# Kernel tuning notes

Measured on AMD Instinct MI355X. Metric: run time of the kernel, lower is better.

## Reference

```python
import jax, jax.numpy as jnp
import numpy as np

B, S, D, H = 16, 512, 768, 12
DH = D // H


def setup_inputs() -> dict:
    key = jax.random.key(0)
    ks = jax.random.split(key, 12)
    hidden_states = jax.random.normal(ks[0], (B, S, D), dtype=jnp.float32)
    # additive padding mask: 0 for valid, -10000 for padded tail tokens
    lengths = jax.random.randint(ks[1], (B,), S // 2, S + 1)
    pad = (jnp.arange(S)[None, :] >= lengths[:, None]).astype(jnp.float32)
    attention_mask = (pad * -10000.0)[:, None, None, :]  # [B,1,1,S]
    # row-stochastic graph prior over codes
    pr = jax.random.uniform(ks[2], (B, S, S), dtype=jnp.float32)
    prior = pr / jnp.sum(pr, axis=-1, keepdims=True)
    s = 0.02
    params = dict(
        Wq=jax.random.normal(ks[3], (D, D)) * s, bq=jnp.zeros((D,)),
        Wk=jax.random.normal(ks[4], (D, D)) * s, bk=jnp.zeros((D,)),
        Wv=jax.random.normal(ks[5], (D, D)) * s, bv=jnp.zeros((D,)),
        Wg=jax.random.normal(ks[6], (D, 2)) * s, bg=jnp.zeros((2,)),
        Wo=jax.random.normal(ks[7], (D, D)) * s, bo=jnp.zeros((D,)),
        gamma=jnp.ones((D,)), beta=jnp.zeros((D,)),
    )
    return dict(hidden_states=hidden_states, attention_mask=attention_mask,
                prior=prior, **params)


def _layer_norm(x, gamma, beta, eps=1e-5):
    mu = jnp.mean(x, axis=-1, keepdims=True)
    var = jnp.mean(jnp.square(x - mu), axis=-1, keepdims=True)
    return (x - mu) * jax.lax.rsqrt(var + eps) * gamma + beta


def reference(hidden_states, attention_mask, prior,
              Wq, bq, Wk, bk, Wv, bv, Wg, bg, Wo, bo, gamma, beta):
    b, s, d = hidden_states.shape
    # project and split heads: [B,S,H,DH]
    q = (hidden_states @ Wq + bq).reshape(b, s, H, DH)
    k = (hidden_states @ Wk + bk).reshape(b, s, H, DH)
    v = (hidden_states @ Wv + bv).reshape(b, s, H, DH)
    scores = jnp.einsum('bshd,bthd->bhst', q, k) / jnp.sqrt(jnp.float32(DH))
    scores = scores + attention_mask  # broadcast [B,1,1,S]
    probs = jax.nn.softmax(scores, axis=-1)  # [B,H,S,S]
    # gate: avg-pool over valid tokens, softmax(linear/2)
    valid = (attention_mask.squeeze((1, 2)) == 0.0).astype(hidden_states.dtype)  # [B,S]
    denom = jnp.maximum(jnp.sum(valid, axis=1, keepdims=True), 1.0)
    h_pool = jnp.sum(hidden_states * valid[:, :, None], axis=1) / denom  # [B,D]
    gate = jax.nn.softmax((h_pool @ Wg + bg) / 2.0, axis=-1)  # [B,2]
    probs = probs * gate[:, 0, None, None, None] + prior[:, None, :, :] * gate[:, 1, None, None, None]
    ctx = jnp.einsum('bhst,bthd->bshd', probs, v).reshape(b, s, d)
    out = jax.nn.relu(ctx @ Wo + bo)
    out = _layer_norm(out + hidden_states, gamma, beta)
    return out
```

## Files before the change

kernel.cpp:

```cpp
#include <hip/hip_runtime.h>

#define NB_ 16
#define S_ 512
#define D_ 768
#define H_ 12
#define DH_ 64
#define QT_ 64
#define KT_ 128
#define LDQ_ 1536

typedef __attribute__((ext_vector_type(8))) short bf16x8;
typedef __attribute__((ext_vector_type(4))) float f32x4;
typedef unsigned short ushort_t;

__device__ __forceinline__ unsigned short f2bf(float f){
  unsigned int u = __float_as_uint(f);
  u += 0x7fffu + ((u >> 16) & 1u);
  return (unsigned short)(u >> 16);
}
__device__ __forceinline__ float bf2f(unsigned short s){
  return __uint_as_float(((unsigned int)s) << 16);
}
__device__ __forceinline__ unsigned int pack2(float a, float b){
  return (unsigned int)f2bf(a) | ((unsigned int)f2bf(b) << 16);
}
__device__ __forceinline__ void gld16(const ushort_t* g, ushort_t* l){
  __builtin_amdgcn_global_load_lds((const __attribute__((address_space(1))) unsigned int*)g,
                                   (__attribute__((address_space(3))) unsigned int*)l, 16, 0, 0);
}

__global__ __launch_bounds__(256) void k_setup(
    const float* __restrict__ hs, const float* __restrict__ mask, const float* __restrict__ prior,
    const float* __restrict__ W0, const float* __restrict__ W1,
    const float* __restrict__ W2, const float* __restrict__ W3,
    const float* __restrict__ b0, const float* __restrict__ b1, const float* __restrict__ b2,
    ushort_t* __restrict__ hsb, ushort_t* __restrict__ wt, float* __restrict__ bqkv,
    float* __restrict__ partial, float* __restrict__ pcnt, ushort_t* __restrict__ priorb)
{
  __shared__ float t[32][33];
  const int bx = blockIdx.x, tid = threadIdx.x;
  if (bx < 512){
    int chunk = bx & 31, b = bx >> 5;
    const float* mrow = mask + b * S_ + chunk * 16;
    const float* base = hs + ((size_t)b * S_ + chunk * 16) * D_;
    ushort_t* obase = hsb + ((size_t)b * S_ + chunk * 16) * D_;
    float a0 = 0.f, a1 = 0.f, a2 = 0.f, cnt = 0.f;
#pragma unroll 2
    for (int s = 0; s < 16; s++){
      const float* r = base + (size_t)s * D_;
      float x0 = r[tid], x1 = r[tid + 256], x2 = r[tid + 512];
      ushort_t* o = obase + (size_t)s * D_;
      o[tid] = f2bf(x0); o[tid + 256] = f2bf(x1); o[tid + 512] = f2bf(x2);
      if (mrow[s] == 0.0f){ a0 += x0; a1 += x1; a2 += x2; cnt += 1.0f; }
    }
    float* o = partial + (size_t)(b * 32 + chunk) * D_;
    o[tid] = a0; o[tid + 256] = a1; o[tid + 512] = a2;
    if (tid == 0) pcnt[b * 32 + chunk] = cnt;
  } else if (bx < 512 + 2304){
    int idx = bx - 512;
    int z = idx / 576, rem = idx - z * 576;
    int ky = rem / 24, nx = rem - ky * 24;
    const float* W = (z == 0) ? W0 : (z == 1) ? W1 : (z == 2) ? W2 : W3;
    ushort_t* o = wt + (size_t)z * D_ * D_;
    int j = tid & 31, i0 = tid >> 5;
    int kb = ky * 32, nb = nx * 32;
#pragma unroll
    for (int r = 0; r < 4; r++){
      int i = i0 + r * 8;
      t[i][j] = W[(size_t)(kb + i) * D_ + nb + j];
    }
    __syncthreads();
#pragma unroll
    for (int r = 0; r < 4; r++){
      int i = i0 + r * 8;
      o[(size_t)(nb + i) * D_ + kb + j] = f2bf(t[j][i]);
    }
  } else if (bx < 2825){
    int i = (bx - 2816) * 256 + tid;
    if (i < 3 * D_){
      float v = (i < D_) ? b0[i] : (i < 2 * D_) ? b1[i - D_] : b2[i - 2 * D_];
      bqkv[i] = v;
    }
  } else {
    size_t i = (size_t)(bx - 2825) * 4096 + (size_t)tid * 16;
    const float4* s4 = (const float4*)(prior + i);
    float4 f0 = s4[0], f1 = s4[1], f2 = s4[2], f3 = s4[3];
    uint4 p0, p1;
    p0.x = pack2(f0.x, f0.y); p0.y = pack2(f0.z, f0.w);
    p0.z = pack2(f1.x, f1.y); p0.w = pack2(f1.z, f1.w);
    p1.x = pack2(f2.x, f2.y); p1.y = pack2(f2.z, f2.w);
    p1.z = pack2(f3.x, f3.y); p1.w = pack2(f3.z, f3.w);
    *(uint4*)(priorb + i) = p0;
    *(uint4*)(priorb + i + 8) = p1;
  }
}

__global__ __launch_bounds__(256, 2) void k_gemm_qkv(
    const ushort_t* __restrict__ Am, const ushort_t* __restrict__ Bm,
    ushort_t* __restrict__ Cq, ushort_t* __restrict__ vtp,
    const float* __restrict__ bias,
    const float* __restrict__ partial, const float* __restrict__ pcnt,
    const float* __restrict__ Wg, const float* __restrict__ bg, float* __restrict__ gate)
{
  __shared__ ushort_t As[2][128 * 64];
  __shared__ ushort_t Bs[2][128 * 64];
  const int tid = threadIdx.x;

  if (blockIdx.y == 18){
    if (blockIdx.x >= 16) return;
    float* red = (float*)As;
    float* hp  = red + 256;
    int b = blockIdx.x;
    float a0 = 0.f, a1 = 0.f, a2 = 0.f;
#pragma unroll
    for (int c = 0; c < 32; c++){
      const float* p = partial + (size_t)(b * 32 + c) * D_;
      a0 += p[tid]; a1 += p[tid + 256]; a2 += p[tid + 512];
    }
    float denom = 0.f;
#pragma unroll
    for (int c = 0; c < 32; c++) denom += pcnt[b * 32 + c];
    float inv = 1.0f / fmaxf(denom, 1.0f);
    hp[tid] = a0 * inv; hp[tid + 256] = a1 * inv; hp[tid + 512] = a2 * inv;
    __syncthreads();
    float p0 = 0.f, p1 = 0.f;
    for (int d = tid; d < D_; d += 256){ p0 += hp[d] * Wg[d * 2]; p1 += hp[d] * Wg[d * 2 + 1]; }
    red[tid] = p0; __syncthreads();
    for (int o = 128; o > 0; o >>= 1){ if (tid < o) red[tid] += red[tid + o]; __syncthreads(); }
    float z0 = red[0]; __syncthreads();
    red[tid] = p1; __syncthreads();
    for (int o = 128; o > 0; o >>= 1){ if (tid < o) red[tid] += red[tid + o]; __syncthreads(); }
    float z1 = red[0];
    if (tid == 0){
      z0 = (z0 + bg[0]) * 0.5f; z1 = (z1 + bg[1]) * 0.5f;
      float m = fmaxf(z0, z1);
      float e0 = __expf(z0 - m), e1 = __expf(z1 - m);
      float ssum = e0 + e1;
      gate[b * 2] = e0 / ssum; gate[b * 2 + 1] = e1 / ssum;
    }
    return;
  }

  const int m0 = blockIdx.x * 128, n0 = blockIdx.y * 128;
  const int wid = tid >> 6, lane = tid & 63;
  const int quad = lane >> 4, l16 = lane & 15;
  const int wm = wid >> 1, wn = wid & 1;
  const int sw = l16 & 7;

  auto stage = [&](int buf, int k0){
#pragma unroll
    for (int c = 0; c < 4; c++){
      int idx = tid + c * 256;
      int row = idx >> 3, p = idx & 7;
      int cg = p ^ (row & 7);
      gld16(Am + (size_t)(m0 + row) * D_ + k0 + cg * 8, &As[buf][idx * 8]);
    }
#pragma unroll
    for (int c = 0; c < 4; c++){
      int idx = tid + c * 256;
      int row = idx >> 3, p = idx & 7;
      int cg = p ^ (row & 7);
      gld16(Bm + (size_t)(n0 + row) * D_ + k0 + cg * 8, &Bs[buf][idx * 8]);
    }
  };

  f32x4 acc[4][4];
#pragma unroll
  for (int i = 0; i < 4; i++)
#pragma unroll
    for (int j = 0; j < 4; j++) acc[i][j] = (f32x4){0.f, 0.f, 0.f, 0.f};

  stage(0, 0);
  int cur = 0;
  for (int k0 = 0; k0 < D_; k0 += 64){
    if (k0 + 64 < D_){
      stage(cur ^ 1, k0 + 64);
      __builtin_amdgcn_sched_barrier(0);
      asm volatile("s_waitcnt vmcnt(8)" ::: "memory");
    } else {
      __builtin_amdgcn_sched_barrier(0);
      asm volatile("s_waitcnt vmcnt(0)" ::: "memory");
    }
    __builtin_amdgcn_sched_barrier(0);
    __builtin_amdgcn_s_barrier();
#pragma unroll
    for (int ks = 0; ks < 2; ks++){
      bf16x8 af[4], bfv[4];
#pragma unroll
      for (int mi = 0; mi < 4; mi++){
        int row = wm * 64 + mi * 16 + l16;
        af[mi] = *(const bf16x8*)(&As[cur][(row * 8 + ((ks * 4 + quad) ^ sw)) * 8]);
      }
#pragma unroll
      for (int ni = 0; ni < 4; ni++){
        int row = wn * 64 + ni * 16 + l16;
        bfv[ni] = *(const bf16x8*)(&Bs[cur][(row * 8 + ((ks * 4 + quad) ^ sw)) * 8]);
      }
      __builtin_amdgcn_s_setprio(1);
#pragma unroll
      for (int mi = 0; mi < 4; mi++)
#pragma unroll
        for (int ni = 0; ni < 4; ni++)
          acc[mi][ni] = __builtin_amdgcn_mfma_f32_16x16x32_bf16(af[mi], bfv[ni], acc[mi][ni], 0, 0, 0);
      __builtin_amdgcn_s_setprio(0);
    }
    __builtin_amdgcn_sched_barrier(0);
    __builtin_amdgcn_s_barrier();
    cur ^= 1;
  }

  if (n0 >= 1536){
    const int bb = m0 >> 9;
#pragma unroll
    for (int mi = 0; mi < 4; mi++){
#pragma unroll
      for (int ni = 0; ni < 4; ni++){
        int col = n0 + wn * 64 + ni * 16 + l16;
        float bcol = bias[col];
        int hh = (col - 1536) >> 6, dh = (col - 1536) & 63;
        int trow = (m0 & 511) + wm * 64 + mi * 16 + quad * 4;
        uint2 pk;
        pk.x = pack2(acc[mi][ni][0] + bcol, acc[mi][ni][1] + bcol);
        pk.y = pack2(acc[mi][ni][2] + bcol, acc[mi][ni][3] + bcol);
        *(uint2*)(vtp + ((size_t)(bb * H_ + hh) * DH_ + dh) * S_ + trow) = pk;
      }
    }
    return;
  }
#pragma unroll
  for (int mi = 0; mi < 4; mi++){
#pragma unroll
    for (int ni = 0; ni < 4; ni++){
      int col = n0 + wn * 64 + ni * 16 + l16;
      float bcol = bias[col];
#pragma unroll
      for (int r = 0; r < 4; r++){
        int row = m0 + wm * 64 + mi * 16 + quad * 4 + r;
        Cq[(size_t)row * LDQ_ + col] = f2bf(acc[mi][ni][r] + bcol);
      }
    }
  }
}

template<int OUTBF16, int RELU, int RESID, int MAP>
__global__ __launch_bounds__(256, 2) void k_gemm_bt(
    const ushort_t* __restrict__ Am, long sA, int lda,
    const ushort_t* __restrict__ Bm, long sB, int ldb,
    void* __restrict__ Cp, long sC, int ldc,
    const float* __restrict__ bias,
    const float* __restrict__ resid, int K)
{
  __shared__ ushort_t As[2][128 * 64];
  __shared__ ushort_t Bs[2][128 * 64];
  int z, bm, bn;
  if (MAP == 2){ z = blockIdx.x; bm = blockIdx.y; bn = blockIdx.z; }
  else if (MAP == 1){ z = blockIdx.z; bm = blockIdx.x; bn = blockIdx.y; }
  else { z = blockIdx.z; bm = blockIdx.y; bn = blockIdx.x; }
  const ushort_t* Ab = Am + (size_t)z * sA;
  const ushort_t* Bb = Bm + (size_t)z * sB;
  const long coff = (long)z * sC;
  const int tid = threadIdx.x;
  const int m0 = bm * 128, n0 = bn * 128;
  const int wid = tid >> 6, lane = tid & 63;
  const int quad = lane >> 4, l16 = lane & 15;
  const int wm = wid >> 1, wn = wid & 1;
  const int sw = l16 & 7;

  auto stage = [&](int buf, int k0){
#pragma unroll
    for (int c = 0; c < 4; c++){
      int idx = tid + c * 256;
      int row = idx >> 3, p = idx & 7;
      int cg = p ^ (row & 7);
      gld16(Ab + (size_t)(m0 + row) * lda + k0 + cg * 8, &As[buf][idx * 8]);
    }
#pragma unroll
    for (int c = 0; c < 4; c++){
      int idx = tid + c * 256;
      int row = idx >> 3, p = idx & 7;
      int cg = p ^ (row & 7);
      gld16(Bb + (size_t)(n0 + row) * ldb + k0 + cg * 8, &Bs[buf][idx * 8]);
    }
  };

  f32x4 acc[4][4];
#pragma unroll
  for (int i = 0; i < 4; i++)
#pragma unroll
    for (int j = 0; j < 4; j++) acc[i][j] = (f32x4){0.f, 0.f, 0.f, 0.f};

  stage(0, 0);
  int cur = 0;
  for (int k0 = 0; k0 < K; k0 += 64){
    if (k0 + 64 < K){
      stage(cur ^ 1, k0 + 64);
      __builtin_amdgcn_sched_barrier(0);
      asm volatile("s_waitcnt vmcnt(8)" ::: "memory");
    } else {
      __builtin_amdgcn_sched_barrier(0);
      asm volatile("s_waitcnt vmcnt(0)" ::: "memory");
    }
    __builtin_amdgcn_sched_barrier(0);
    __builtin_amdgcn_s_barrier();
#pragma unroll
    for (int ks = 0; ks < 2; ks++){
      bf16x8 af[4], bfv[4];
#pragma unroll
      for (int mi = 0; mi < 4; mi++){
        int row = wm * 64 + mi * 16 + l16;
        af[mi] = *(const bf16x8*)(&As[cur][(row * 8 + ((ks * 4 + quad) ^ sw)) * 8]);
      }
#pragma unroll
      for (int ni = 0; ni < 4; ni++){
        int row = wn * 64 + ni * 16 + l16;
        bfv[ni] = *(const bf16x8*)(&Bs[cur][(row * 8 + ((ks * 4 + quad) ^ sw)) * 8]);
      }
      __builtin_amdgcn_s_setprio(1);
#pragma unroll
      for (int mi = 0; mi < 4; mi++)
#pragma unroll
        for (int ni = 0; ni < 4; ni++)
          acc[mi][ni] = __builtin_amdgcn_mfma_f32_16x16x32_bf16(af[mi], bfv[ni], acc[mi][ni], 0, 0, 0);
      __builtin_amdgcn_s_setprio(0);
    }
    __builtin_amdgcn_sched_barrier(0);
    __builtin_amdgcn_s_barrier();
    cur ^= 1;
  }

#pragma unroll
  for (int mi = 0; mi < 4; mi++){
#pragma unroll
    for (int ni = 0; ni < 4; ni++){
      int col = n0 + wn * 64 + ni * 16 + l16;
      float bcol = bias ? bias[col] : 0.0f;
#pragma unroll
      for (int r = 0; r < 4; r++){
        int row = m0 + wm * 64 + mi * 16 + quad * 4 + r;
        float v = acc[mi][ni][r] + bcol;
        if (RELU) v = fmaxf(v, 0.0f);
        if (RESID) v += resid[(size_t)row * ldc + col];
        long idx = coff + (long)row * ldc + col;
        if (OUTBF16) ((ushort_t*)Cp)[idx] = f2bf(v);
        else         ((float*)Cp)[idx] = v;
      }
    }
  }
}

__global__ __launch_bounds__(256) void k_flash(
    const ushort_t* __restrict__ qkv,
    const ushort_t* __restrict__ vt,
    const ushort_t* __restrict__ priorctx,
    const float* __restrict__ mask,
    const float* __restrict__ gate,
    ushort_t* __restrict__ ctx)
{
  __shared__ ushort_t Ks[KT_ * 64];
  __shared__ ushort_t Vs[DH_ * 128];
  __shared__ ushort_t Ps[QT_ * 128];
  __shared__ float rs[QT_];
  const int z = blockIdx.x, b = z / H_, h = z - b * H_;
  const int q0 = blockIdx.y * QT_;
  const int tid = threadIdx.x;
  const int wid = tid >> 6, lane = tid & 63, quad = lane >> 4, l16 = lane & 15;

  bf16x8 bq[4][2];
#pragma unroll
  for (int ni = 0; ni < 4; ni++)
#pragma unroll
    for (int ks = 0; ks < 2; ks++)
      bq[ni][ks] = *(const bf16x8*)(qkv + ((size_t)(b * S_ + q0 + ni * 16 + l16)) * LDQ_
                                    + h * DH_ + ks * 32 + quad * 8);
  if (tid < QT_) rs[tid] = 0.f;

  f32x4 accv[4];
#pragma unroll
  for (int ni = 0; ni < 4; ni++) accv[ni] = (f32x4){0.f, 0.f, 0.f, 0.f};

  for (int t0 = 0; t0 < S_; t0 += KT_){
    if (mask[b * S_ + t0] != 0.0f) break;
#pragma unroll
    for (int c = 0; c < 4; c++){
      int idx = tid + c * 256;
      int row = idx >> 3, p = idx & 7;
      int cg = p ^ (row & 7);
      gld16(qkv + ((size_t)(b * S_ + t0 + row)) * LDQ_ + D_ + h * DH_ + cg * 8, &Ks[idx * 8]);
    }
#pragma unroll
    for (int c = 0; c < 4; c++){
      int idx = tid + c * 256;
      int row = idx >> 4, p = idx & 15;
      int cg = p ^ (row & 15);
      gld16(vt + (size_t)z * (DH_ * S_) + (size_t)row * S_ + t0 + cg * 8, &Vs[idx * 8]);
    }
    __syncthreads();

    f32x4 accs[2][4];
#pragma unroll
    for (int mi = 0; mi < 2; mi++)
#pragma unroll
      for (int ni = 0; ni < 4; ni++) accs[mi][ni] = (f32x4){0.f, 0.f, 0.f, 0.f};
#pragma unroll
    for (int ks = 0; ks < 2; ks++){
      bf16x8 ak[2];
#pragma unroll
      for (int mi = 0; mi < 2; mi++){
        int row = wid * 32 + mi * 16 + l16;
        ak[mi] = *(const bf16x8*)(&Ks[(row * 8 + ((ks * 4 + quad) ^ (l16 & 7))) * 8]);
      }
#pragma unroll
      for (int mi = 0; mi < 2; mi++)
#pragma unroll
        for (int ni = 0; ni < 4; ni++)
          accs[mi][ni] = __builtin_amdgcn_mfma_f32_16x16x32_bf16(ak[mi], bq[ni][ks], accs[mi][ni], 0, 0, 0);
    }

    float mv[2][4];
#pragma unroll
    for (int mi = 0; mi < 2; mi++)
#pragma unroll
      for (int r = 0; r < 4; r++)
        mv[mi][r] = mask[b * S_ + t0 + wid * 32 + mi * 16 + quad * 4 + r];
    float rowpart[4] = {0.f, 0.f, 0.f, 0.f};
#pragma unroll
    for (int mi = 0; mi < 2; mi++){
      int cw = wid * 4 + mi * 2 + (quad >> 1);
      int off = (quad & 1) * 4;
#pragma unroll
      for (int ni = 0; ni < 4; ni++){
        float e0 = __expf(accs[mi][ni][0] * 0.125f + mv[mi][0]);
        float e1 = __expf(accs[mi][ni][1] * 0.125f + mv[mi][1]);
        float e2 = __expf(accs[mi][ni][2] * 0.125f + mv[mi][2]);
        float e3 = __expf(accs[mi][ni][3] * 0.125f + mv[mi][3]);
        rowpart[ni] += (e0 + e1) + (e2 + e3);
        uint2 pk;
        pk.x = pack2(e0, e1);
        pk.y = pack2(e2, e3);
        *(uint2*)(&Ps[(ni * 16 + l16) * 128 + ((cw ^ (l16 & 7)) * 8 + off)]) = pk;
      }
    }
#pragma unroll
    for (int ni = 0; ni < 4; ni++){
      rowpart[ni] += __shfl_xor(rowpart[ni], 16);
      rowpart[ni] += __shfl_xor(rowpart[ni], 32);
    }
    if (lane < 16){
#pragma unroll
      for (int ni = 0; ni < 4; ni++) atomicAdd(&rs[ni * 16 + l16], rowpart[ni]);
    }
    __syncthreads();

#pragma unroll
    for (int ks = 0; ks < 4; ks++){
      bf16x8 ap = *(const bf16x8*)(&Ps[(wid * 16 + l16) * 128 + ((ks * 4 + quad) ^ (l16 & 7)) * 8]);
#pragma unroll
      for (int ni = 0; ni < 4; ni++){
        bf16x8 bv8 = *(const bf16x8*)(&Vs[((ni * 16 + l16) * 16 + ((ks * 4 + quad) ^ l16)) * 8]);
        accv[ni] = __builtin_amdgcn_mfma_f32_16x16x32_bf16(ap, bv8, accv[ni], 0, 0, 0);
      }
    }
    __syncthreads();
  }

  const float g0 = gate[b * 2], g1 = gate[b * 2 + 1];
#pragma unroll
  for (int ni = 0; ni < 4; ni++){
#pragma unroll
    for (int r = 0; r < 4; r++){
      int q = wid * 16 + quad * 4 + r;
      int dh = ni * 16 + l16;
      float scl = g0 / rs[q];
      size_t idx = ((size_t)(b * S_ + q0 + q)) * D_ + h * DH_ + dh;
      float v = accv[ni][r] * scl + g1 * bf2f(priorctx[idx]);
      ctx[idx] = f2bf(v);
    }
  }
}

__global__ __launch_bounds__(256) void k_ln(float* __restrict__ out, const float* __restrict__ gamma,
                                            const float* __restrict__ beta){
  __shared__ float red[256];
  int row = blockIdx.x, tid = threadIdx.x;
  float* p = out + (size_t)row * D_;
  float x0 = p[tid], x1 = p[tid + 256], x2 = p[tid + 512];
  red[tid] = x0 + x1 + x2; __syncthreads();
  for (int o = 128; o > 0; o >>= 1){ if (tid < o) red[tid] += red[tid + o]; __syncthreads(); }
  float mu = red[0] * (1.0f / 768.0f);
  __syncthreads();
  float d0 = x0 - mu, d1 = x1 - mu, d2 = x2 - mu;
  red[tid] = d0 * d0 + d1 * d1 + d2 * d2; __syncthreads();
  for (int o = 128; o > 0; o >>= 1){ if (tid < o) red[tid] += red[tid + o]; __syncthreads(); }
  float rsv = rsqrtf(red[0] * (1.0f / 768.0f) + 1e-5f);
  p[tid]       = d0 * rsv * gamma[tid]       + beta[tid];
  p[tid + 256] = d1 * rsv * gamma[tid + 256] + beta[tid + 256];
  p[tid + 512] = d2 * rsv * gamma[tid + 512] + beta[tid + 512];
}

extern "C" void kernel_launch(void* const* d_in, const int* in_sizes, int n_in,
                              void* d_out, int out_size, void* d_ws, size_t ws_size,
                              hipStream_t stream){
  const float* hs    = (const float*)d_in[0];
  const float* mask  = (const float*)d_in[1];
  const float* prior = (const float*)d_in[2];
  const float* Wq = (const float*)d_in[3];  const float* bq = (const float*)d_in[4];
  const float* Wk = (const float*)d_in[5];  const float* bk = (const float*)d_in[6];
  const float* Wv = (const float*)d_in[7];  const float* bv = (const float*)d_in[8];
  const float* Wg = (const float*)d_in[9];  const float* bg = (const float*)d_in[10];
  const float* Wo = (const float*)d_in[11]; const float* bo = (const float*)d_in[12];
  const float* gamma = (const float*)d_in[13]; const float* beta = (const float*)d_in[14];
  float* out = (float*)d_out;

  size_t off = 0;
  auto alloc = [&](size_t bytes) -> char* {
    char* p = (char*)d_ws + off;
    off += (bytes + 255) & ~(size_t)255;
    return p;
  };
  const size_t HSD = (size_t)NB_ * S_ * D_;
  ushort_t* hsb     = (ushort_t*)alloc(HSD * 2);
  ushort_t* qkvb    = (ushort_t*)alloc(HSD * 2 * 2);
  ushort_t* vtb     = (ushort_t*)alloc(HSD * 2);
  ushort_t* wt      = (ushort_t*)alloc((size_t)4 * D_ * D_ * 2);
  ushort_t* priorctx= (ushort_t*)alloc(HSD * 2);
  ushort_t* ctx     = (ushort_t*)alloc(HSD * 2);
  float*    bqkv    = (float*)alloc((size_t)3 * D_ * 4);
  float*    gate    = (float*)alloc(256);
  float*    partial = (float*)alloc((size_t)NB_ * 32 * D_ * 4);
  float*    pcnt    = (float*)alloc((size_t)NB_ * 32 * 4);
  ushort_t* priorb  = ctx;

  k_setup<<<dim3(3849), 256, 0, stream>>>(hs, mask, prior, Wq, Wk, Wv, Wo, bq, bk, bv,
                                          hsb, wt, bqkv, partial, pcnt, priorb);
  k_gemm_qkv<<<dim3(64, 19), 256, 0, stream>>>(hsb, wt, qkvb, vtb, bqkv,
                                               partial, pcnt, Wg, bg, gate);
  k_gemm_bt<1, 0, 0, 2><<<dim3(16, 4, 6), 256, 0, stream>>>(
      priorb, (long)S_ * S_, S_, vtb, (long)H_ * DH_ * S_, S_,
      priorctx, (long)S_ * D_, D_, nullptr, nullptr, S_);
  k_flash<<<dim3(NB_ * H_, S_ / QT_), 256, 0, stream>>>(
      qkvb, vtb, priorctx, mask, gate, ctx);
  k_gemm_bt<0, 1, 1, 1><<<dim3(64, 6, 1), 256, 0, stream>>>(
      ctx, 0, D_, wt + 3 * (size_t)D_ * D_, 0, D_, out, 0, D_, bo, hs, D_);
  k_ln<<<dim3(NB_ * S_), 256, 0, stream>>>(out, gamma, beta);
}
```

Before: 254.6 us.

## Fuse prior@V product into flash attention kernel, drop separate prior GEMM

Removes the standalone batched GEMM that computed prior·V into a priorctx buffer. The flash kernel now also loads prior tiles into the K shared buffer and accumulates prior·V in a second MFMA accumulator set. It does this for all key tiles, including the masked tail, which previously ended the loop early. This saves a kernel launch and the priorctx write and read. In exchange, the flash kernel does more work per block, and V tiles must now be loaded for padded tiles too.

Result: no change. 252.6 us (-0.8%).

```diff
diff --git a/kernel.cpp b/kernel.cpp
--- a/kernel.cpp
+++ b/kernel.cpp
@@ -17,9 +17,6 @@
   unsigned int u = __float_as_uint(f);
   u += 0x7fffu + ((u >> 16) & 1u);
   return (unsigned short)(u >> 16);
-}
-__device__ __forceinline__ float bf2f(unsigned short s){
-  return __uint_as_float(((unsigned int)s) << 16);
 }
 __device__ __forceinline__ unsigned int pack2(float a, float b){
   return (unsigned int)f2bf(a) | ((unsigned int)f2bf(b) << 16);
@@ -351,7 +348,7 @@
 __global__ __launch_bounds__(256) void k_flash(
     const ushort_t* __restrict__ qkv,
     const ushort_t* __restrict__ vt,
-    const ushort_t* __restrict__ priorctx,
+    const ushort_t* __restrict__ priorb,
     const float* __restrict__ mask,
     const float* __restrict__ gate,
     ushort_t* __restrict__ ctx)
@@ -374,19 +371,15 @@
                                     + h * DH_ + ks * 32 + quad * 8);
   if (tid < QT_) rs[tid] = 0.f;
 
-  f32x4 accv[4];
-#pragma unroll
-  for (int ni = 0; ni < 4; ni++) accv[ni] = (f32x4){0.f, 0.f, 0.f, 0.f};
+  f32x4 accv[4], accp[4];
+#pragma unroll
+  for (int ni = 0; ni < 4; ni++){
+    accv[ni] = (f32x4){0.f, 0.f, 0.f, 0.f};
+    accp[ni] = (f32x4){0.f, 0.f, 0.f, 0.f};
+  }
 
   for (int t0 = 0; t0 < S_; t0 += KT_){
-    if (mask[b * S_ + t0] != 0.0f) break;
-#pragma unroll
-    for (int c = 0; c < 4; c++){
-      int idx = tid + c * 256;
-      int row = idx >> 3, p = idx & 7;
-      int cg = p ^ (row & 7);
-      gld16(qkv + ((size_t)(b * S_ + t0 + row)) * LDQ_ + D_ + h * DH_ + cg * 8, &Ks[idx * 8]);
-    }
+    const bool live = (mask[b * S_ + t0] == 0.0f);
 #pragma unroll
     for (int c = 0; c < 4; c++){
       int idx = tid + c * 256;
@@ -394,70 +387,107 @@
       int cg = p ^ (row & 15);
       gld16(vt + (size_t)z * (DH_ * S_) + (size_t)row * S_ + t0 + cg * 8, &Vs[idx * 8]);
     }
-    __syncthreads();
-
-    f32x4 accs[2][4];
-#pragma unroll
-    for (int mi = 0; mi < 2; mi++)
-#pragma unroll
-      for (int ni = 0; ni < 4; ni++) accs[mi][ni] = (f32x4){0.f, 0.f, 0.f, 0.f};
-#pragma unroll
-    for (int ks = 0; ks < 2; ks++){
-      bf16x8 ak[2];
+    if (live){
+#pragma unroll
+      for (int c = 0; c < 4; c++){
+        int idx = tid + c * 256;
+        int row = idx >> 3, p = idx & 7;
+        int cg = p ^ (row & 7);
+        gld16(qkv + ((size_t)(b * S_ + t0 + row)) * LDQ_ + D_ + h * DH_ + cg * 8, &Ks[idx * 8]);
+      }
+      __syncthreads();
+
+      f32x4 accs[2][4];
+#pragma unroll
+      for (int mi = 0; mi < 2; mi++)
+#pragma unroll
+        for (int ni = 0; ni < 4; ni++) accs[mi][ni] = (f32x4){0.f, 0.f, 0.f, 0.f};
+#pragma unroll
+      for (int ks = 0; ks < 2; ks++){
+        bf16x8 ak[2];
+#pragma unroll
+        for (int mi = 0; mi < 2; mi++){
+          int row = wid * 32 + mi * 16 + l16;
+          ak[mi] = *(const bf16x8*)(&Ks[(row * 8 + ((ks * 4 + quad) ^ (l16 & 7))) * 8]);
+        }
+#pragma unroll
+        for (int mi = 0; mi < 2; mi++)
+#pragma unroll
+          for (int ni = 0; ni < 4; ni++)
+            accs[mi][ni] = __builtin_amdgcn_mfma_f32_16x16x32_bf16(ak[mi], bq[ni][ks], accs[mi][ni], 0, 0, 0);
+      }
+
+      float mv[2][4];
+#pragma unroll
+      for (int mi = 0; mi < 2; mi++)
+#pragma unroll
+        for (int r = 0; r < 4; r++)
+          mv[mi][r] = mask[b * S_ + t0 + wid * 32 + mi * 16 + quad * 4 + r];
+      float rowpart[4] = {0.f, 0.f, 0.f, 0.f};
 #pragma unroll
       for (int mi = 0; mi < 2; mi++){
-        int row = wid * 32 + mi * 16 + l16;
-        ak[mi] = *(const bf16x8*)(&Ks[(row * 8 + ((ks * 4 + quad) ^ (l16 & 7))) * 8]);
-      }
-#pragma unroll
-      for (int mi = 0; mi < 2; mi++)
-#pragma unroll
-        for (int ni = 0; ni < 4; ni++)
-          accs[mi][ni] = __builtin_amdgcn_mfma_f32_16x16x32_bf16(ak[mi], bq[ni][ks], accs[mi][ni], 0, 0, 0);
-    }
-
-    float mv[2][4];
-#pragma unroll
-    for (int mi = 0; mi < 2; mi++)
-#pragma unroll
-      for (int r = 0; r < 4; r++)
-        mv[mi][r] = mask[b * S_ + t0 + wid * 32 + mi * 16 + quad * 4 + r];
-    float rowpart[4] = {0.f, 0.f, 0.f, 0.f};
-#pragma unroll
-    for (int mi = 0; mi < 2; mi++){
-      int cw = wid * 4 + mi * 2 + (quad >> 1);
-      int off = (quad & 1) * 4;
+        int cw = wid * 4 + mi * 2 + (quad >> 1);
+        int off = (quad & 1) * 4;
+#pragma unroll
+        for (int ni = 0; ni < 4; ni++){
+          float e0 = __expf(accs[mi][ni][0] * 0.125f + mv[mi][0]);
+          float e1 = __expf(accs[mi][ni][1] * 0.125f + mv[mi][1]);
+          float e2 = __expf(accs[mi][ni][2] * 0.125f + mv[mi][2]);
+          float e3 = __expf(accs[mi][ni][3] * 0.125f + mv[mi][3]);
+          rowpart[ni] += (e0 + e1) + (e2 + e3);
+          uint2 pk;
+          pk.x = pack2(e0, e1);
+          pk.y = pack2(e2, e3);
+          *(uint2*)(&Ps[(ni * 16 + l16) * 128 + ((cw ^ (l16 & 7)) * 8 + off)]) = pk;
+        }
+      }
 #pragma unroll
       for (int ni = 0; ni < 4; ni++){
-        float e0 = __expf(accs[mi][ni][0] * 0.125f + mv[mi][0]);
-        float e1 = __expf(accs[mi][ni][1] * 0.125f + mv[mi][1]);
-        float e2 = __expf(accs[mi][ni][2] * 0.125f + mv[mi][2]);
-        float e3 = __expf(accs[mi][ni][3] * 0.125f + mv[mi][3]);
-        rowpart[ni] += (e0 + e1) + (e2 + e3);
-        uint2 pk;
-        pk.x = pack2(e0, e1);
-        pk.y = pack2(e2, e3);
-        *(uint2*)(&Ps[(ni * 16 + l16) * 128 + ((cw ^ (l16 & 7)) * 8 + off)]) = pk;
-      }
-    }
-#pragma unroll
-    for (int ni = 0; ni < 4; ni++){
-      rowpart[ni] += __shfl_xor(rowpart[ni], 16);
-      rowpart[ni] += __shfl_xor(rowpart[ni], 32);
-    }
-    if (lane < 16){
-#pragma unroll
-      for (int ni = 0; ni < 4; ni++) atomicAdd(&rs[ni * 16 + l16], rowpart[ni]);
-    }
-    __syncthreads();
+        rowpart[ni] += __shfl_xor(rowpart[ni], 16);
+        rowpart[ni] += __shfl_xor(rowpart[ni], 32);
+      }
+      if (lane < 16){
+#pragma unroll
+        for (int ni = 0; ni < 4; ni++) atomicAdd(&rs[ni * 16 + l16], rowpart[ni]);
+      }
+      __syncthreads();
+
+#pragma unroll
+      for (int c = 0; c < 4; c++){
+        int idx = tid + c * 256;
+        int row = idx >> 4, p = idx & 15;
+        int cg = p ^ (row & 15);
+        gld16(priorb + ((size_t)(b * S_ + q0 + row)) * S_ + t0 + cg * 8, &Ks[idx * 8]);
+      }
+
+#pragma unroll
+      for (int ks = 0; ks < 4; ks++){
+        bf16x8 ap = *(const bf16x8*)(&Ps[(wid * 16 + l16) * 128 + ((ks * 4 + quad) ^ (l16 & 7)) * 8]);
+#pragma unroll
+        for (int ni = 0; ni < 4; ni++){
+          bf16x8 bv8 = *(const bf16x8*)(&Vs[((ni * 16 + l16) * 16 + ((ks * 4 + quad) ^ l16)) * 8]);
+          accv[ni] = __builtin_amdgcn_mfma_f32_16x16x32_bf16(ap, bv8, accv[ni], 0, 0, 0);
+        }
+      }
+      __syncthreads();
+    } else {
+#pragma unroll
+      for (int c = 0; c < 4; c++){
+        int idx = tid + c * 256;
+        int row = idx >> 4, p = idx & 15;
+        int cg = p ^ (row & 15);
+        gld16(priorb + ((size_t)(b * S_ + q0 + row)) * S_ + t0 + cg * 8, &Ks[idx * 8]);
+      }
+      __syncthreads();
+    }
 
 #pragma unroll
     for (int ks = 0; ks < 4; ks++){
-      bf16x8 ap = *(const bf16x8*)(&Ps[(wid * 16 + l16) * 128 + ((ks * 4 + quad) ^ (l16 & 7)) * 8]);
+      bf16x8 apr = *(const bf16x8*)(&Ks[((wid * 16 + l16) * 16 + ((ks * 4 + quad) ^ l16)) * 8]);
 #pragma unroll
       for (int ni = 0; ni < 4; ni++){
         bf16x8 bv8 = *(const bf16x8*)(&Vs[((ni * 16 + l16) * 16 + ((ks * 4 + quad) ^ l16)) * 8]);
-        accv[ni] = __builtin_amdgcn_mfma_f32_16x16x32_bf16(ap, bv8, accv[ni], 0, 0, 0);
+        accp[ni] = __builtin_amdgcn_mfma_f32_16x16x32_bf16(apr, bv8, accp[ni], 0, 0, 0);
       }
     }
     __syncthreads();
@@ -472,7 +502,7 @@
       int dh = ni * 16 + l16;
       float scl = g0 / rs[q];
       size_t idx = ((size_t)(b * S_ + q0 + q)) * D_ + h * DH_ + dh;
-      float v = accv[ni][r] * scl + g1 * bf2f(priorctx[idx]);
+      float v = accv[ni][r] * scl + g1 * accp[ni][r];
       ctx[idx] = f2bf(v);
     }
   }
@@ -522,23 +552,19 @@
   ushort_t* qkvb    = (ushort_t*)alloc(HSD * 2 * 2);
   ushort_t* vtb     = (ushort_t*)alloc(HSD * 2);
   ushort_t* wt      = (ushort_t*)alloc((size_t)4 * D_ * D_ * 2);
-  ushort_t* priorctx= (ushort_t*)alloc(HSD * 2);
+  ushort_t* priorb  = (ushort_t*)alloc((size_t)NB_ * S_ * S_ * 2);
   ushort_t* ctx     = (ushort_t*)alloc(HSD * 2);
   float*    bqkv    = (float*)alloc((size_t)3 * D_ * 4);
   float*    gate    = (float*)alloc(256);
   float*    partial = (float*)alloc((size_t)NB_ * 32 * D_ * 4);
   float*    pcnt    = (float*)alloc((size_t)NB_ * 32 * 4);
-  ushort_t* priorb  = ctx;
 
   k_setup<<<dim3(3849), 256, 0, stream>>>(hs, mask, prior, Wq, Wk, Wv, Wo, bq, bk, bv,
                                           hsb, wt, bqkv, partial, pcnt, priorb);
   k_gemm_qkv<<<dim3(64, 19), 256, 0, stream>>>(hsb, wt, qkvb, vtb, bqkv,
                                                partial, pcnt, Wg, bg, gate);
-  k_gemm_bt<1, 0, 0, 2><<<dim3(16, 4, 6), 256, 0, stream>>>(
-      priorb, (long)S_ * S_, S_, vtb, (long)H_ * DH_ * S_, S_,
-      priorctx, (long)S_ * D_, D_, nullptr, nullptr, S_);
   k_flash<<<dim3(NB_ * H_, S_ / QT_), 256, 0, stream>>>(
-      qkvb, vtb, priorctx, mask, gate, ctx);
+      qkvb, vtb, priorb, mask, gate, ctx);
   k_gemm_bt<0, 1, 1, 1><<<dim3(64, 6, 1), 256, 0, stream>>>(
       ctx, 0, D_, wt + 3 * (size_t)D_ * D_, 0, D_, out, 0, D_, bo, hs, D_);
   k_ln<<<dim3(NB_ * S_), 256, 0, stream>>>(out, gamma, beta);
```
